# Kernel tuning notes

Measured on AMD Instinct MI355X. Metric: run time of the kernel, lower is better.

Reference implementation:

```python
import jax, jax.numpy as jnp
import numpy as np

B = 262144          # batch
D = 128             # feature / hidden width (cfg ind/outd)
OUT = 1             # last layer outd
NE = 5              # five treatment-range experts Q1..Q5
PT = np.array([0.0, 0.2, 0.4, 0.6, 0.8, 1.0], dtype=np.float32)


def setup_inputs() -> dict:
    key = jax.random.key(0)
    ks = jax.random.split(key, 10)
    # x[:,0] = treatment in [0,1), x[:,1:] = features (uniform, matching torch.rand init scale)
    x = jax.random.uniform(ks[0], (B, 1 + D), dtype=jnp.float32)
    # expert params, stacked over the 5 experts; torch init is rand(0,1)
    u = lambda k, shp: jax.random.uniform(k, shp, dtype=jnp.float32)
    return {
        "x": x,
        "W1": u(ks[1], (NE, D, D)),   "tw1": u(ks[2], (NE, 1, D)),   "b1": u(ks[3], (NE, D)),
        "W2": u(ks[4], (NE, D, D)),   "tw2": u(ks[5], (NE, 1, D)),   "b2": u(ks[6], (NE, D)),
        "W3": u(ks[7], (NE, D, OUT)), "tw3": u(ks[8], (NE, 1, OUT)), "b3": u(ks[9], (NE, OUT)),
    }


def reference(x, W1, tw1, b1, W2, tw2, b2, W3, tw3, b3):
    t = x[:, :1]          # [B,1] treatment
    f = x[:, 1:]          # [B,D] features
    out = jnp.zeros((x.shape[0], OUT), dtype=x.dtype)
    for e in range(NE):
        # routing mask: pt[e] <= t < pt[e+1]
        mask = (t >= PT[e]) & (t < PT[e + 1])          # [B,1]
        # expert MLP (Treat_Linear stack): out = f@W + t@tw + b, relu except last
        h = jax.nn.relu(f @ W1[e] + t @ tw1[e] + b1[e])
        h = jax.nn.relu(h @ W2[e] + t @ tw2[e] + b2[e])
        o = h @ W3[e] + t @ tw3[e] + b3[e]             # last layer, no act
        out = out + jnp.where(mask, o, jnp.zeros((), x.dtype))
    return out
```

## Files before the change

kernel.cpp:

```cpp
#include <hip/hip_runtime.h>

#define NROWS 262144
#define NE 5
#define CAP 57344
#define NCH 4096
#define BPE 51
#define CHUNK 256
#define CPAD 16

typedef __attribute__((ext_vector_type(8))) short short8;
typedef __attribute__((ext_vector_type(8))) unsigned short ushort8;
typedef __attribute__((ext_vector_type(4))) float f32x4;
typedef __attribute__((ext_vector_type(4), aligned(4))) float f32x4u;

__device__ __forceinline__ unsigned short f2bf(float x) {
  unsigned u = __float_as_uint(x);
  u += 0x7FFF + ((u >> 16) & 1);
  return (unsigned short)(u >> 16);
}
__device__ __forceinline__ int eclass(float t) {
  return (t >= 0.2f) + (t >= 0.4f) + (t >= 0.6f) + (t >= 0.8f);
}

__global__ __launch_bounds__(256) void convw(const float* __restrict__ W1,
                                             const float* __restrict__ W2,
                                             unsigned short* __restrict__ Wswz) {
  int idx = blockIdx.x * 256 + threadIdx.x;
  int which = idx / 81920;
  int rem = idx % 81920;
  int e = rem / 16384;
  int jk = rem % 16384;
  int j = jk >> 7;
  int k = jk & 127;
  const float* W = which ? W2 : W1;
  int byteoff = (j * 256 + k * 2) ^ ((j & 7) << 4);
  Wswz[(size_t)e * 32768 + which * 16384 + (byteoff >> 1)] =
      f2bf(W[(size_t)e * 16384 + k * 128 + j]);
}

__global__ __launch_bounds__(256) void thist(const float* __restrict__ x,
                                             float* __restrict__ tcomp,
                                             int* __restrict__ hist) {
  __shared__ int hS[4][NE];
  int tid = threadIdx.x;
  int r = blockIdx.x * 256 + tid;
  if (tid < 20) hS[tid / NE][tid % NE] = 0;
  float t = x[(size_t)r * 129];
  int e = eclass(t);
  tcomp[r] = t;
  __syncthreads();
  atomicAdd(&hS[tid >> 6][e], 1);
  __syncthreads();
  if (tid < 20) {
    int sub = tid / NE, ee = tid % NE;
    hist[ee * NCH + blockIdx.x * 4 + sub] = hS[sub][ee];
  }
}

__global__ __launch_bounds__(256) void scan(const int* __restrict__ hist,
                                            int* __restrict__ boff,
                                            int* __restrict__ cnt) {
  __shared__ int wsum[4];
  int e = blockIdx.x;
  int tid = threadIdx.x;
  int lane = tid & 63, wv = tid >> 6;

  int v[16];
  int s = 0;
  const int* h = hist + e * NCH + tid * 16;
#pragma unroll
  for (int j = 0; j < 16; ++j) { v[j] = h[j]; s += v[j]; }

  int sc = s;
#pragma unroll
  for (int off = 1; off < 64; off <<= 1) {
    int nv = __shfl_up(sc, off);
    if (lane >= off) sc += nv;
  }
  if (lane == 63) wsum[wv] = sc;
  __syncthreads();
  int wexc = 0;
  for (int k = 0; k < wv; ++k) wexc += wsum[k];
  int run = wexc + sc - s;
  int* bo = boff + e * NCH + tid * 16;
#pragma unroll
  for (int j = 0; j < 16; ++j) { bo[j] = run; run += v[j]; }
  if (tid == 255) cnt[e * CPAD] = run;
}

__global__ __launch_bounds__(256) void perm(const float* __restrict__ tcomp,
                                            const int* __restrict__ boff,
                                            float* __restrict__ tcb,
                                            int* __restrict__ ridb,
                                            int* __restrict__ dstperm) {
  __shared__ int lc[4][NE];
  int tid = threadIdx.x;
  int blk = blockIdx.x;
  int r = blk * 256 + tid;
  int sub = tid >> 6;
  if (tid < 20) lc[tid / NE][tid % NE] = 0;
  float t = tcomp[r];
  int e = eclass(t);
  __syncthreads();
  int lp = atomicAdd(&lc[sub][e], 1);
  int d = e * CAP + min(boff[e * NCH + blk * 4 + sub] + lp, CAP - 1);
  tcb[d] = t;
  ridb[d] = r;
  dstperm[r] = d;
}

__global__ __launch_bounds__(256) void compact2(
    const float* __restrict__ x, const int* __restrict__ dstperm,
    unsigned short* __restrict__ xc) {
  int tid = threadIdx.x;
  int r = blockIdx.x * 8 + (tid >> 5);
  int k = tid & 31;
  int d = dstperm[r];
  f32x4u v = *(const f32x4u*)(x + (size_t)r * 129 + 1 + k * 4);
  unsigned long long p =
      (unsigned long long)f2bf(v[0]) |
      ((unsigned long long)f2bf(v[1]) << 16) |
      ((unsigned long long)f2bf(v[2]) << 32) |
      ((unsigned long long)f2bf(v[3]) << 48);
  *(unsigned long long*)(xc + (size_t)d * 128 + k * 4) = p;
}

__global__ __launch_bounds__(512, 2) void mlp(
    const unsigned short* __restrict__ xc, const float* __restrict__ tcb,
    const int* __restrict__ ridb, const int* __restrict__ cnt,
    const unsigned short* __restrict__ Wswz,
    const float* __restrict__ tw1, const float* __restrict__ b1,
    const float* __restrict__ tw2, const float* __restrict__ b2,
    const float* __restrict__ W3, const float* __restrict__ tw3,
    const float* __restrict__ b3, float* __restrict__ out) {
  __shared__ unsigned short wl[32768];
  __shared__ unsigned short h1[8][32 * 128];

  int tid = threadIdx.x;
  int e = blockIdx.x / BPE;
  int bi = blockIdx.x % BPE;
  int n = min(cnt[e * CPAD], CAP);

  {
    const ushort8* wsrc = (const ushort8*)(Wswz + (size_t)e * 32768);
    ushort8* wdst = (ushort8*)wl;
#pragma unroll
    for (int i = 0; i < 8; ++i) wdst[i * 512 + tid] = wsrc[i * 512 + tid];
  }
  __syncthreads();

  int wave = tid >> 6;
  int lane = tid & 63;
  int lr = lane & 15;
  int lq = lane >> 4;

  const char* wp1 = (const char*)wl;
  const char* wp2 = (const char*)wl + 32768;
  char* hp = (char*)h1[wave];
  const unsigned short* xce = xc + (size_t)e * CAP * 128;
  const float* tce = tcb + (size_t)e * CAP;
  const int* ride = ridb + (size_t)e * CAP;

  int nchunk = (n + CHUNK - 1) / CHUNK;

  auto loada = [&](int cc, short8 (&pa0)[4], short8 (&pa1)[4],
                   float& ptv, int& prv) {
    int base = cc * CHUNK + wave * 32;
    int ci = min(base + (lane & 31), n - 1);
    ptv = tce[ci];
    prv = ride[ci];
    int row0 = min(base + lr, n - 1);
    int row1 = min(base + 16 + lr, n - 1);
#pragma unroll
    for (int ks = 0; ks < 4; ++ks) {
      pa0[ks] = *(const short8*)(xce + (size_t)row0 * 128 + ks * 32 + lq * 8);
      pa1[ks] = *(const short8*)(xce + (size_t)row1 * 128 + ks * 32 + lq * 8);
    }
  };

  short8 a0[4], a1[4];
  float tv; int rv;
  int c = bi;
  if (c < nchunk) loada(c, a0, a1, tv, rv);

  for (; c < nchunk; ) {
    int cn = c + BPE;
    bool hn = (cn < nchunk);
    short8 na0[4], na1[4];
    float ntv = 0.f; int nrv = 0;
    if (hn) loada(cn, na0, na1, ntv, nrv);

    int base = c * CHUNK + wave * 32;

    float t0[4], t1[4];
    int ro0[4], ro1[4];
#pragma unroll
    for (int rr = 0; rr < 4; ++rr) {
      t0[rr] = __shfl(tv, lq * 4 + rr);
      t1[rr] = __shfl(tv, 16 + lq * 4 + rr);
      ro0[rr] = __shfl(rv, lq * 4 + rr);
      ro1[rr] = __shfl(rv, 16 + lq * 4 + rr);
    }

#pragma unroll
    for (int ct = 0; ct < 8; ++ct) {
      int col = ct * 16 + lr;
      short8 b[4];
#pragma unroll
      for (int ks = 0; ks < 4; ++ks) {
        int bo = (col * 256 + ks * 64 + lq * 16) ^ ((lr & 7) << 4);
        b[ks] = *(const short8*)(wp1 + bo);
      }
      f32x4 acc0 = {0.f, 0.f, 0.f, 0.f};
      f32x4 acc1 = {0.f, 0.f, 0.f, 0.f};
#pragma unroll
      for (int ks = 0; ks < 4; ++ks) {
        acc0 = __builtin_amdgcn_mfma_f32_16x16x32_bf16(a0[ks], b[ks], acc0, 0, 0, 0);
        acc1 = __builtin_amdgcn_mfma_f32_16x16x32_bf16(a1[ks], b[ks], acc1, 0, 0, 0);
      }
      float twv = tw1[e * 128 + col];
      float bv  = b1[e * 128 + col];
#pragma unroll
      for (int rr = 0; rr < 4; ++rr) {
        int r0_ = lq * 4 + rr;
        int r1_ = r0_ + 16;
        float v0 = fmaxf(acc0[rr] + t0[rr] * twv + bv, 0.f);
        float v1 = fmaxf(acc1[rr] + t1[rr] * twv + bv, 0.f);
        *(unsigned short*)(hp + ((r0_ * 256 + col * 2) ^ ((r0_ & 7) << 4))) = f2bf(v0);
        *(unsigned short*)(hp + ((r1_ * 256 + col * 2) ^ ((r1_ & 7) << 4))) = f2bf(v1);
      }
    }

    asm volatile("s_waitcnt lgkmcnt(0)" ::: "memory");
    __builtin_amdgcn_sched_barrier(0);

#pragma unroll
    for (int ks = 0; ks < 4; ++ks) {
      int off0 = (lr * 256 + ks * 64 + lq * 16) ^ ((lr & 7) << 4);
      int off1 = ((16 + lr) * 256 + ks * 64 + lq * 16) ^ ((lr & 7) << 4);
      a0[ks] = *(const short8*)(hp + off0);
      a1[ks] = *(const short8*)(hp + off1);
    }

    const float* W3e = W3 + e * 128;
    float o0[4] = {0.f, 0.f, 0.f, 0.f};
    float o1[4] = {0.f, 0.f, 0.f, 0.f};
#pragma unroll
    for (int ct = 0; ct < 8; ++ct) {
      int col = ct * 16 + lr;
      short8 b[4];
#pragma unroll
      for (int ks = 0; ks < 4; ++ks) {
        int bo = (col * 256 + ks * 64 + lq * 16) ^ ((lr & 7) << 4);
        b[ks] = *(const short8*)(wp2 + bo);
      }
      f32x4 acc0 = {0.f, 0.f, 0.f, 0.f};
      f32x4 acc1 = {0.f, 0.f, 0.f, 0.f};
#pragma unroll
      for (int ks = 0; ks < 4; ++ks) {
        acc0 = __builtin_amdgcn_mfma_f32_16x16x32_bf16(a0[ks], b[ks], acc0, 0, 0, 0);
        acc1 = __builtin_amdgcn_mfma_f32_16x16x32_bf16(a1[ks], b[ks], acc1, 0, 0, 0);
      }
      float twv = tw2[e * 128 + col];
      float bv  = b2[e * 128 + col];
      float w3v = W3e[col];
#pragma unroll
      for (int rr = 0; rr < 4; ++rr) {
        float v0 = fmaxf(acc0[rr] + t0[rr] * twv + bv, 0.f);
        float v1 = fmaxf(acc1[rr] + t1[rr] * twv + bv, 0.f);
        o0[rr] += v0 * w3v;
        o1[rr] += v1 * w3v;
      }
    }

#pragma unroll
    for (int rr = 0; rr < 4; ++rr) {
      float s0 = o0[rr], s1 = o1[rr];
      s0 += __shfl_xor(s0, 1);  s1 += __shfl_xor(s1, 1);
      s0 += __shfl_xor(s0, 2);  s1 += __shfl_xor(s1, 2);
      s0 += __shfl_xor(s0, 4);  s1 += __shfl_xor(s1, 4);
      s0 += __shfl_xor(s0, 8);  s1 += __shfl_xor(s1, 8);
      o0[rr] = s0;  o1[rr] = s1;
    }

    if (lr == 0) {
      float tw3v = tw3[e];
      float b3v  = b3[e];
#pragma unroll
      for (int rr = 0; rr < 4; ++rr) {
        if (base + lq * 4 + rr < n)
          out[ro0[rr]] = o0[rr] + t0[rr] * tw3v + b3v;
        if (base + 16 + lq * 4 + rr < n)
          out[ro1[rr]] = o1[rr] + t1[rr] * tw3v + b3v;
      }
    }

    if (hn) {
#pragma unroll
      for (int ks = 0; ks < 4; ++ks) { a0[ks] = na0[ks]; a1[ks] = na1[ks]; }
      tv = ntv; rv = nrv;
    }
    c = cn;
  }
}

extern "C" void kernel_launch(void* const* d_in, const int* in_sizes, int n_in,
                              void* d_out, int out_size, void* d_ws, size_t ws_size,
                              hipStream_t stream) {
  const float* x   = (const float*)d_in[0];
  const float* W1  = (const float*)d_in[1];
  const float* tw1 = (const float*)d_in[2];
  const float* b1  = (const float*)d_in[3];
  const float* W2  = (const float*)d_in[4];
  const float* tw2 = (const float*)d_in[5];
  const float* b2  = (const float*)d_in[6];
  const float* W3  = (const float*)d_in[7];
  const float* tw3 = (const float*)d_in[8];
  const float* b3  = (const float*)d_in[9];
  float* out = (float*)d_out;

  char* ws = (char*)d_ws;
  size_t off = 0;
  int*   cnt     = (int*)(ws + off);   off += 1024;
  float* tcomp   = (float*)(ws + off); off += (size_t)NROWS * 4;
  int*   hist    = (int*)(ws + off);   off += (size_t)NE * NCH * 4;
  int*   boff    = (int*)(ws + off);   off += (size_t)NE * NCH * 4;
  int*   dstperm = (int*)(ws + off);   off += (size_t)NROWS * 4;
  int*   ridb    = (int*)(ws + off);   off += (size_t)NE * CAP * 4;
  float* tcb     = (float*)(ws + off); off += (size_t)NE * CAP * 4;
  unsigned short* xc = (unsigned short*)(ws + off); off += (size_t)NE * CAP * 256;
  unsigned short* Wswz = (unsigned short*)(ws + off);

  convw<<<640, 256, 0, stream>>>(W1, W2, Wswz);
  thist<<<NROWS / 256, 256, 0, stream>>>(x, tcomp, hist);
  scan<<<NE, 256, 0, stream>>>(hist, boff, cnt);
  perm<<<NROWS / 256, 256, 0, stream>>>(tcomp, boff, tcb, ridb, dstperm);
  compact2<<<NROWS / 8, 256, 0, stream>>>(x, dstperm, xc);
  mlp<<<NE * BPE, 512, 0, stream>>>(xc, tcb, ridb, cnt, Wswz,
                                    tw1, b1, tw2, b2, W3, tw3, b3, out);
}
```

Baseline: 88.91 us.

## Fuse weight conversion into histogram and merge permutation with row compaction

```diff
diff --git a/kernel.cpp b/kernel.cpp
--- a/kernel.cpp
+++ b/kernel.cpp
@@ -3,7 +3,7 @@
 #define NROWS 262144
 #define NE 5
 #define CAP 57344
-#define NCH 4096
+#define NCH 8192
 #define BPE 51
 #define CHUNK 256
 #define CPAD 16
@@ -22,45 +22,45 @@
   return (t >= 0.2f) + (t >= 0.4f) + (t >= 0.6f) + (t >= 0.8f);
 }
 
-__global__ __launch_bounds__(256) void convw(const float* __restrict__ W1,
-                                             const float* __restrict__ W2,
-                                             unsigned short* __restrict__ Wswz) {
-  int idx = blockIdx.x * 256 + threadIdx.x;
-  int which = idx / 81920;
-  int rem = idx % 81920;
-  int e = rem / 16384;
-  int jk = rem % 16384;
-  int j = jk >> 7;
-  int k = jk & 127;
-  const float* W = which ? W2 : W1;
-  int byteoff = (j * 256 + k * 2) ^ ((j & 7) << 4);
-  Wswz[(size_t)e * 32768 + which * 16384 + (byteoff >> 1)] =
-      f2bf(W[(size_t)e * 16384 + k * 128 + j]);
-}
-
-__global__ __launch_bounds__(256) void thist(const float* __restrict__ x,
-                                             float* __restrict__ tcomp,
-                                             int* __restrict__ hist) {
-  __shared__ int hS[4][NE];
+__global__ __launch_bounds__(256) void thist_convw(
+    const float* __restrict__ x,
+    const float* __restrict__ W1, const float* __restrict__ W2,
+    unsigned short* __restrict__ Wswz, int* __restrict__ hist) {
+  __shared__ int hS[8][NE];
   int tid = threadIdx.x;
-  int r = blockIdx.x * 256 + tid;
-  if (tid < 20) hS[tid / NE][tid % NE] = 0;
+  int blk = blockIdx.x;
+
+  int idx = blk * 256 + tid;
+  if (idx < 163840) {
+    int which = idx / 81920;
+    int rem = idx % 81920;
+    int e = rem / 16384;
+    int jk = rem % 16384;
+    int j = jk >> 7;
+    int k = jk & 127;
+    const float* W = which ? W2 : W1;
+    int byteoff = (j * 256 + k * 2) ^ ((j & 7) << 4);
+    Wswz[(size_t)e * 32768 + which * 16384 + (byteoff >> 1)] =
+        f2bf(W[(size_t)e * 16384 + k * 128 + j]);
+  }
+
+  if (tid < 40) hS[tid / NE][tid % NE] = 0;
+  int r = blk * 256 + tid;
   float t = x[(size_t)r * 129];
   int e = eclass(t);
-  tcomp[r] = t;
-  __syncthreads();
-  atomicAdd(&hS[tid >> 6][e], 1);
-  __syncthreads();
-  if (tid < 20) {
+  __syncthreads();
+  atomicAdd(&hS[tid >> 5][e], 1);
+  __syncthreads();
+  if (tid < 40) {
     int sub = tid / NE, ee = tid % NE;
-    hist[ee * NCH + blockIdx.x * 4 + sub] = hS[sub][ee];
-  }
-}
-
-__global__ __launch_bounds__(256) void scan(const int* __restrict__ hist,
+    hist[ee * NCH + blk * 8 + sub] = hS[sub][ee];
+  }
+}
+
+__global__ __launch_bounds__(512) void scan(const int* __restrict__ hist,
                                             int* __restrict__ boff,
                                             int* __restrict__ cnt) {
-  __shared__ int wsum[4];
+  __shared__ int wsum[8];
   int e = blockIdx.x;
   int tid = threadIdx.x;
   int lane = tid & 63, wv = tid >> 6;
@@ -85,38 +85,43 @@
   int* bo = boff + e * NCH + tid * 16;
 #pragma unroll
   for (int j = 0; j < 16; ++j) { bo[j] = run; run += v[j]; }
-  if (tid == 255) cnt[e * CPAD] = run;
-}
-
-__global__ __launch_bounds__(256) void perm(const float* __restrict__ tcomp,
-                                            const int* __restrict__ boff,
-                                            float* __restrict__ tcb,
-                                            int* __restrict__ ridb,
-                                            int* __restrict__ dstperm) {
-  __shared__ int lc[4][NE];
+  if (tid == 511) cnt[e * CPAD] = run;
+}
+
+__global__ __launch_bounds__(1024) void compact3(
+    const float* __restrict__ x, const int* __restrict__ boff,
+    unsigned short* __restrict__ xc, float* __restrict__ tcb,
+    int* __restrict__ ridb) {
+  __shared__ int lcS[NE];
+  __shared__ int dstS[32];
+
   int tid = threadIdx.x;
+  int row = tid >> 5;
+  int k = tid & 31;
   int blk = blockIdx.x;
-  int r = blk * 256 + tid;
-  int sub = tid >> 6;
-  if (tid < 20) lc[tid / NE][tid % NE] = 0;
-  float t = tcomp[r];
-  int e = eclass(t);
-  __syncthreads();
-  int lp = atomicAdd(&lc[sub][e], 1);
-  int d = e * CAP + min(boff[e * NCH + blk * 4 + sub] + lp, CAP - 1);
-  tcb[d] = t;
-  ridb[d] = r;
-  dstperm[r] = d;
-}
-
-__global__ __launch_bounds__(256) void compact2(
-    const float* __restrict__ x, const int* __restrict__ dstperm,
-    unsigned short* __restrict__ xc) {
-  int tid = threadIdx.x;
-  int r = blockIdx.x * 8 + (tid >> 5);
-  int k = tid & 31;
-  int d = dstperm[r];
+  int r = blk * 32 + row;
+
+  if (tid < NE) lcS[tid] = 0;
+
   f32x4u v = *(const f32x4u*)(x + (size_t)r * 129 + 1 + k * 4);
+
+  float t = 0.f;
+  int e = 0;
+  if (k == 0) {
+    t = x[(size_t)r * 129];
+    e = eclass(t);
+  }
+  __syncthreads();
+  if (k == 0) {
+    int lp = atomicAdd(&lcS[e], 1);
+    int d = e * CAP + min(boff[e * NCH + blk] + lp, CAP - 1);
+    dstS[row] = d;
+    tcb[d] = t;
+    ridb[d] = r;
+  }
+  __syncthreads();
+
+  int d = dstS[row];
   unsigned long long p =
       (unsigned long long)f2bf(v[0]) |
       ((unsigned long long)f2bf(v[1]) << 16) |
@@ -321,21 +326,17 @@
 
   char* ws = (char*)d_ws;
   size_t off = 0;
-  int*   cnt     = (int*)(ws + off);   off += 1024;
-  float* tcomp   = (float*)(ws + off); off += (size_t)NROWS * 4;
-  int*   hist    = (int*)(ws + off);   off += (size_t)NE * NCH * 4;
-  int*   boff    = (int*)(ws + off);   off += (size_t)NE * NCH * 4;
-  int*   dstperm = (int*)(ws + off);   off += (size_t)NROWS * 4;
-  int*   ridb    = (int*)(ws + off);   off += (size_t)NE * CAP * 4;
-  float* tcb     = (float*)(ws + off); off += (size_t)NE * CAP * 4;
+  int*   cnt  = (int*)(ws + off);   off += 1024;
+  int*   hist = (int*)(ws + off);   off += (size_t)NE * NCH * 4;
+  int*   boff = (int*)(ws + off);   off += (size_t)NE * NCH * 4;
+  int*   ridb = (int*)(ws + off);   off += (size_t)NE * CAP * 4;
+  float* tcb  = (float*)(ws + off); off += (size_t)NE * CAP * 4;
   unsigned short* xc = (unsigned short*)(ws + off); off += (size_t)NE * CAP * 256;
   unsigned short* Wswz = (unsigned short*)(ws + off);
 
-  convw<<<640, 256, 0, stream>>>(W1, W2, Wswz);
-  thist<<<NROWS / 256, 256, 0, stream>>>(x, tcomp, hist);
-  scan<<<NE, 256, 0, stream>>>(hist, boff, cnt);
-  perm<<<NROWS / 256, 256, 0, stream>>>(tcomp, boff, tcb, ridb, dstperm);
-  compact2<<<NROWS / 8, 256, 0, stream>>>(x, dstperm, xc);
+  thist_convw<<<NROWS / 256, 256, 0, stream>>>(x, W1, W2, Wswz, hist);
+  scan<<<NE, 512, 0, stream>>>(hist, boff, cnt);
+  compact3<<<NROWS / 32, 1024, 0, stream>>>(x, boff, xc, tcb, ridb);
   mlp<<<NE * BPE, 512, 0, stream>>>(xc, tcb, ridb, cnt, Wswz,
                                     tw1, b1, tw2, b2, W3, tw3, b3, out);
 }
```

New measurement: 85.46 us. 1.04x faster.
